# Kernel tuning notes

Measured on AMD Instinct MI355X. Metric: run time of the kernel, lower is better.

Reference implementation:

```python
import jax, jax.numpy as jnp
import numpy as np

NUM_HEADS = 16
LAMBDA = 0.1
HADAMARD_SCALE = 0.05
ROPE_BASE = 10000.0


def _rope(t):
    # t: [B, H, S, hd] -- rotary embedding (half-split convention)
    hd = t.shape[-1]
    S = t.shape[2]
    half = hd // 2
    inv_freq = 1.0 / (ROPE_BASE ** (jnp.arange(half, dtype=jnp.float32) / half))
    ang = jnp.arange(S, dtype=jnp.float32)[:, None] * inv_freq[None, :]  # [S, half]
    cos = jnp.cos(ang).astype(t.dtype)
    sin = jnp.sin(ang).astype(t.dtype)
    t1, t2 = t[..., :half], t[..., half:]
    return jnp.concatenate([t1 * cos - t2 * sin, t2 * cos + t1 * sin], axis=-1)


def _rotate_half(t):
    half = t.shape[-1] // 2
    return jnp.concatenate([-t[..., half:], t[..., :half]], axis=-1)


def setup_inputs() -> dict:
    key = jax.random.key(0)
    ks = jax.random.split(key, 6)
    B, S, D = 2, 2048, 1024
    scale = 1.0 / np.sqrt(D).astype(np.float32)
    x = jax.random.normal(ks[0], (B, S, D), jnp.float32)
    Wq = jax.random.normal(ks[1], (D, D), jnp.float32) * scale
    Wk = jax.random.normal(ks[2], (D, D), jnp.float32) * scale
    Wv = jax.random.normal(ks[3], (D, D), jnp.float32) * scale
    Wo = jax.random.normal(ks[4], (D, D), jnp.float32) * scale
    gate_w = jax.random.normal(ks[5], (D // NUM_HEADS,), jnp.float32) * 0.01
    return {"x": x, "Wq": Wq, "Wk": Wk, "Wv": Wv, "Wo": Wo, "gate_w": gate_w}


def reference(x, Wq, Wk, Wv, Wo, gate_w):
    B, S, D = x.shape
    H = NUM_HEADS
    hd = D // H

    def heads(W):
        return (x @ W.T).reshape(B, S, H, hd).transpose(0, 2, 1, 3)  # [B,H,S,hd]

    Q = _rope(heads(Wq))
    K = _rope(heads(Wk))
    V = heads(Wv)

    causal = jnp.tril(jnp.ones((S, S), dtype=bool))
    inv_sqrt_d = 1.0 / jnp.sqrt(jnp.asarray(hd, x.dtype))

    def attend(q, k):
        # first-order + lambda * second-order (elementwise-squared) scores
        s = (jnp.einsum('bhsd,bhtd->bhst', q, k)
             + LAMBDA * jnp.einsum('bhsd,bhtd->bhst', q * q, k * k)) * inv_sqrt_d
        s = jnp.where(causal, s, jnp.asarray(-1e9, s.dtype))
        a = jax.nn.softmax(s, axis=-1)
        return jnp.einsum('bhst,bhtd->bhsd', a, V)

    out1 = attend(Q, K)                                  # standard pass
    out2 = attend(_rotate_half(Q), _rotate_half(K))      # rotated second pass

    # hadamard gate mix of the two passes
    out = 0.5 * (out1 + out2) + HADAMARD_SCALE * (out1 * out2) * gate_w

    out = out.transpose(0, 2, 1, 3).reshape(B, S, D)
    return out @ Wo.T
```

## Files before the change

kernel.cpp:

```cpp
#include <hip/hip_runtime.h>

typedef unsigned short u16;
typedef __attribute__((ext_vector_type(4))) unsigned short u16x4;
typedef __attribute__((ext_vector_type(8))) unsigned short u16x8;
typedef __attribute__((ext_vector_type(8))) short s16x8;
typedef __attribute__((ext_vector_type(4))) float f32x4;

__device__ __forceinline__ u16 f2bf(float f) {
  unsigned int u = __float_as_uint(f);
  u += 0x7FFFu + ((u >> 16) & 1u);
  return (u16)(u >> 16);
}
__device__ __forceinline__ float bf2f(u16 h) {
  return __uint_as_float(((unsigned int)h) << 16);
}

__device__ __forceinline__ void gload_lds16(const u16* g, u16* l) {
  __builtin_amdgcn_global_load_lds(
      (const __attribute__((address_space(1))) unsigned int*)(g),
      (__attribute__((address_space(3))) unsigned int*)(l), 16, 0, 0);
}

__global__ __launch_bounds__(256) void cvt_all(const float* __restrict__ x,
                                               const float* __restrict__ Wq,
                                               const float* __restrict__ Wk,
                                               const float* __restrict__ Wv,
                                               const float* __restrict__ Wo,
                                               u16* __restrict__ xbf,
                                               u16* __restrict__ wbf,
                                               u16* __restrict__ wobf) {
  int blk = blockIdx.x;
  const float* src;
  u16* dst;
  int i;
  if (blk < 4096) {
    src = x; dst = xbf; i = blk * 256 + threadIdx.x;
  } else {
    int wb = blk - 4096;
    int sel = wb >> 10;
    src = (sel == 0) ? Wq : (sel == 1) ? Wk : (sel == 2) ? Wv : Wo;
    dst = (sel < 3) ? (wbf + (size_t)sel * 1048576) : wobf;
    i = (wb & 1023) * 256 + threadIdx.x;
  }
  float4 v = reinterpret_cast<const float4*>(src)[i];
  u16x4 o;
  o.x = f2bf(v.x); o.y = f2bf(v.y); o.z = f2bf(v.z); o.w = f2bf(v.w);
  reinterpret_cast<u16x4*>(dst)[i] = o;
}

__device__ __forceinline__ void store_out(float* p, float v) { *p = v; }
__device__ __forceinline__ void store_out(u16* p, float v) { *p = f2bf(v); }

template <typename OutT, int WM, int WN>
__global__ __launch_bounds__(256) void gemm_bt(const u16* __restrict__ A,
                                               const u16* __restrict__ Bw,
                                               OutT* __restrict__ C, int N, int K) {
  __shared__ u16 As[2][WM * 1024];
  __shared__ u16 Bs[2][WN * 1024];
  const int tid = threadIdx.x;
  const int lane = tid & 63;
  const int wave = tid >> 6;
  const int wm = wave >> 1, wn = wave & 1;
  const int lh = lane & 15, quad = lane >> 4;
  const int q8 = quad * 8;
  const int m0 = blockIdx.y * (WM * 32), n0 = blockIdx.x * (WN * 32);
  constexpr int NCH = 2 * (WM + WN);
  constexpr int PER = NCH / 4;

  auto stage = [&](int buf, int kt) {
    const int kb = kt * 32;
#pragma unroll
    for (int i = 0; i < PER; ++i) {
      const int c = wave * PER + i;
      if (c < 2 * WM) {
        gload_lds16(A + (size_t)(m0 + c * 16 + lh) * K + kb + q8,
                    &As[buf][c * 512 + lane * 8]);
      } else {
        const int rb = c - 2 * WM;
        gload_lds16(Bw + (size_t)(n0 + rb * 16 + lh) * K + kb + q8,
                    &Bs[buf][rb * 512 + lane * 8]);
      }
    }
  };

  f32x4 acc[WM][WN];
#pragma unroll
  for (int i = 0; i < WM; ++i)
#pragma unroll
    for (int j = 0; j < WN; ++j) { acc[i][j][0] = 0.f; acc[i][j][1] = 0.f; acc[i][j][2] = 0.f; acc[i][j][3] = 0.f; }

  const int nkt = K >> 5;
  stage(0, 0);
  __syncthreads();
  for (int kt = 0; kt < nkt; ++kt) {
    const int p = kt & 1;
    if (kt < nkt - 1) stage(1 - p, kt + 1);
    s16x8 af[WM], bf4[WN];
#pragma unroll
    for (int mb = 0; mb < WM; ++mb)
      af[mb] = *reinterpret_cast<const s16x8*>(&As[p][(wm * WM + mb) * 512 + lane * 8]);
#pragma unroll
    for (int nb = 0; nb < WN; ++nb)
      bf4[nb] = *reinterpret_cast<const s16x8*>(&Bs[p][(wn * WN + nb) * 512 + lane * 8]);
#pragma unroll
    for (int mb = 0; mb < WM; ++mb)
#pragma unroll
      for (int nb = 0; nb < WN; ++nb)
        acc[mb][nb] = __builtin_amdgcn_mfma_f32_16x16x32_bf16(af[mb], bf4[nb], acc[mb][nb], 0, 0, 0);
    __syncthreads();
  }
#pragma unroll
  for (int mb = 0; mb < WM; ++mb)
#pragma unroll
    for (int nb = 0; nb < WN; ++nb) {
      const int col = n0 + wn * (WN * 16) + nb * 16 + lh;
#pragma unroll
      for (int r = 0; r < 4; ++r) {
        const int row = m0 + wm * (WM * 16) + mb * 16 + quad * 4 + r;
        store_out(&C[(size_t)row * N + col], acc[mb][nb][r]);
      }
    }
}

__global__ __launch_bounds__(256) void qkv_gemm(const u16* __restrict__ A,
                                                const u16* __restrict__ Bw,
                                                u16* __restrict__ Vt,
                                                u16* __restrict__ Qs,
                                                u16* __restrict__ Kb,
                                                u16* __restrict__ K2b) {
  __shared__ u16 As[2][4096];
  __shared__ u16 Bs[2][4096];
  const int tid = threadIdx.x;
  const int lane = tid & 63;
  const int wave = tid >> 6;
  const int wm = wave >> 1, wn = wave & 1;
  const int lh = lane & 15, quad = lane >> 4;
  const int q8 = quad * 8;
  const int bx = blockIdx.x;
  const int m0 = blockIdx.y * 128, n0 = bx * 128;
  const int K = 1024;

  auto stage = [&](int buf, int kt) {
    const int kb = kt * 32;
#pragma unroll
    for (int i = 0; i < 4; ++i) {
      const int c = wave * 4 + i;
      if (c < 8) {
        gload_lds16(A + (size_t)(m0 + c * 16 + lh) * K + kb + q8,
                    &As[buf][c * 512 + lane * 8]);
      } else {
        const int rb = c - 8;
        gload_lds16(Bw + (size_t)(n0 + rb * 16 + lh) * K + kb + q8,
                    &Bs[buf][rb * 512 + lane * 8]);
      }
    }
  };

  f32x4 acc[4][4];
#pragma unroll
  for (int i = 0; i < 4; ++i)
#pragma unroll
    for (int j = 0; j < 4; ++j) { acc[i][j][0] = 0.f; acc[i][j][1] = 0.f; acc[i][j][2] = 0.f; acc[i][j][3] = 0.f; }

  stage(0, 0);
  __syncthreads();
  for (int kt = 0; kt < 32; ++kt) {
    const int p = kt & 1;
    if (kt < 31) stage(1 - p, kt + 1);
    s16x8 af[4], bf4[4];
#pragma unroll
    for (int mb = 0; mb < 4; ++mb)
      af[mb] = *reinterpret_cast<const s16x8*>(&As[p][(wm * 4 + mb) * 512 + lane * 8]);
#pragma unroll
    for (int nb = 0; nb < 4; ++nb)
      bf4[nb] = *reinterpret_cast<const s16x8*>(&Bs[p][(wn * 4 + nb) * 512 + lane * 8]);
#pragma unroll
    for (int mb = 0; mb < 4; ++mb)
#pragma unroll
      for (int nb = 0; nb < 4; ++nb)
        acc[mb][nb] = __builtin_amdgcn_mfma_f32_16x16x32_bf16(af[mb], bf4[nb], acc[mb][nb], 0, 0, 0);
    __syncthreads();
  }

  if (bx < 16) {
    const bool isQ = (bx < 8);
#pragma unroll
    for (int nb = 0; nb < 2; ++nb) {
      const int d = nb * 16 + lh;
      const float invf = __expf((float)d * -0.2878231366f);
      const int col = n0 + wn * 64 + nb * 16 + lh;
      const int ch = col & 1023;
      const int h = ch >> 6;
#pragma unroll
      for (int mb = 0; mb < 4; ++mb)
#pragma unroll
        for (int r = 0; r < 4; ++r) {
          const int row = m0 + wm * 64 + mb * 16 + quad * 4 + r;
          const int s = row & 2047, b = row >> 11;
          float ang = (float)s * invf;
          float sv, cv;
          __sincosf(ang, &sv, &cv);
          const float v1 = acc[mb][nb][r], v2 = acc[mb][nb + 2][r];
          const float e0 = v1 * cv - v2 * sv;
          const float e1 = v2 * cv + v1 * sv;
          const size_t ofs = (size_t)((b * 16 + h) * 2048 + s) * 64 + d;
          if (isQ) {
            Qs[ofs]      = f2bf(e0 * 0.125f);
            Qs[ofs + 32] = f2bf(e1 * 0.125f);
          } else {
            Kb[ofs]       = f2bf(e0);
            Kb[ofs + 32]  = f2bf(e1);
            K2b[ofs]      = f2bf(e0 * e0);
            K2b[ofs + 32] = f2bf(e1 * e1);
          }
        }
    }
  } else {
#pragma unroll
    for (int mb = 0; mb < 4; ++mb)
#pragma unroll
      for (int nb = 0; nb < 4; ++nb) {
        const int col = n0 + wn * 64 + nb * 16 + lh;
        const int ch = col & 1023;
        const int h = ch >> 6, d = ch & 63;
        const int row0 = m0 + wm * 64 + mb * 16 + quad * 4;
        const int s0 = row0 & 2047, b = row0 >> 11;
        u16x4 o;
#pragma unroll
        for (int r = 0; r < 4; ++r) o[r] = f2bf(acc[mb][nb][r]);
        *reinterpret_cast<u16x4*>(Vt + (size_t)((b * 16 + h) * 64 + d) * 2048 + s0) = o;
      }
  }
}

__global__ __launch_bounds__(256, 2) void attn_kernel(const u16* __restrict__ Qs,
                                                      const u16* __restrict__ Kb,
                                                      const u16* __restrict__ K2b,
                                                      const u16* __restrict__ Vt,
                                                      const float* __restrict__ gate,
                                                      u16* __restrict__ attn,
                                                      float* __restrict__ Opart,
                                                      float* __restrict__ Lpart,
                                                      float* __restrict__ Opart2,
                                                      float* __restrict__ Lpart2) {
  const int lin = blockIdx.y * 44 + blockIdx.x;
  const int xcd = lin & 7;
  const int slot = lin >> 3;
  const int bh = xcd * 4 + (slot / 44);
  const int bxv = slot % 44;

  int qi, kt0, kt1, chunk, which;
  bool split;
  if (bxv < 32) {
    qi = 15 - (bxv >> 2); chunk = bxv & 3; split = true; which = 0;
    const int T = 4 * qi + 4;
    kt0 = (chunk * T) >> 2;
    kt1 = (((chunk + 1) * T) >> 2) - 1;
  } else if (bxv < 40) {
    const int t = bxv - 32;
    qi = 7 - (t >> 1); chunk = t & 1; split = true; which = 1;
    const int nk = 2 * qi + 2; kt0 = chunk * nk; kt1 = kt0 + nk - 1;
  } else {
    qi = 43 - bxv; split = false; which = 0; chunk = 0; kt0 = 0; kt1 = 4 * qi + 3;
  }
  const int tid = threadIdx.x, lane = tid & 63, wave = tid >> 6;
  const int lh = lane & 15, quad = lane >> 4;
  const int b = bh >> 4, h = bh & 15;
  __shared__ u16 stageS[2][4096];
  __shared__ u16 Pbuf[4][640];
  const int base = qi * 128 + wave * 32;
  const int q8 = quad * 8;

  auto do_stage = [&](int buf, int kt) {
#pragma unroll
    for (int i = 0; i < 2; ++i) {
      const int c = wave * 2 + i;
      const int t2 = c >> 2, f = c & 3, kk = f >> 1, nb = f & 1;
      const u16* src = (t2 ? K2b : Kb) +
          (size_t)(bh * 2048 + kt * 32 + nb * 16 + lh) * 64 + kk * 32 + q8;
      gload_lds16(src, &stageS[buf][t2 * 2048 + f * 512 + lane * 8]);
    }
  };

  s16x8 qf[2][2], q2f[2][2];
#pragma unroll
  for (int mb = 0; mb < 2; ++mb) {
    const size_t qoff = (size_t)(bh * 2048 + base + mb * 16 + lh) * 64 + q8;
#pragma unroll
    for (int kk = 0; kk < 2; ++kk) {
      qf[mb][kk] = *reinterpret_cast<const s16x8*>(Qs + qoff + kk * 32);
#pragma unroll
      for (int j = 0; j < 8; ++j) {
        float f = bf2f((u16)qf[mb][kk][j]);
        q2f[mb][kk][j] = (short)f2bf(f * f * 0.8f);
      }
    }
  }

  const u16* Vbase = Vt + (size_t)bh * 131072;

  f32x4 oacc[2][4];
  float lsum[2][4];
#pragma unroll
  for (int mb = 0; mb < 2; ++mb)
#pragma unroll
    for (int nb = 0; nb < 4; ++nb) { oacc[mb][nb][0] = 0.f; oacc[mb][nb][1] = 0.f; oacc[mb][nb][2] = 0.f; oacc[mb][nb][3] = 0.f; }
#pragma unroll
  for (int mb = 0; mb < 2; ++mb)
#pragma unroll
    for (int r = 0; r < 4; ++r) lsum[mb][r] = 0.f;

  do_stage(0, kt0);
  __syncthreads();

  const int wmaxrow = base + 31;
  for (int kt = kt0; kt <= kt1; ++kt) {
    const int p = (kt - kt0) & 1;
    if (kt < kt1) do_stage(1 - p, kt + 1);

    if (kt * 32 <= wmaxrow) {
      const u16* Ks = stageS[p];
      f32x4 sacc[2][2];
#pragma unroll
      for (int mb = 0; mb < 2; ++mb)
#pragma unroll
        for (int nb = 0; nb < 2; ++nb) { sacc[mb][nb][0] = -8.f; sacc[mb][nb][1] = -8.f; sacc[mb][nb][2] = -8.f; sacc[mb][nb][3] = -8.f; }
      __builtin_amdgcn_s_setprio(1);
#pragma unroll
      for (int nb = 0; nb < 2; ++nb)
#pragma unroll
        for (int kk = 0; kk < 2; ++kk) {
          s16x8 kf  = *reinterpret_cast<const s16x8*>(&Ks[(kk * 2 + nb) * 512 + lane * 8]);
          s16x8 k2f = *reinterpret_cast<const s16x8*>(&Ks[2048 + (kk * 2 + nb) * 512 + lane * 8]);
#pragma unroll
          for (int mb = 0; mb < 2; ++mb) {
            sacc[mb][nb] = __builtin_amdgcn_mfma_f32_16x16x32_bf16(qf[mb][kk],  kf,  sacc[mb][nb], 0, 0, 0);
            sacc[mb][nb] = __builtin_amdgcn_mfma_f32_16x16x32_bf16(q2f[mb][kk], k2f, sacc[mb][nb], 0, 0, 0);
          }
        }
      __builtin_amdgcn_s_setprio(0);

      s16x8 vf[4];
#pragma unroll
      for (int nb = 0; nb < 4; ++nb)
        vf[nb] = *reinterpret_cast<const s16x8*>(
            Vbase + (size_t)(nb * 16 + lh) * 2048 + kt * 32 + q8);

      if (kt * 32 + 31 > base) {
#pragma unroll
        for (int mb = 0; mb < 2; ++mb)
#pragma unroll
          for (int nb = 0; nb < 2; ++nb) {
            const int colg = kt * 32 + nb * 16 + lh;
#pragma unroll
            for (int r = 0; r < 4; ++r) {
              const int rowg = base + mb * 16 + quad * 4 + r;
              if (colg > rowg) sacc[mb][nb][r] = -1e9f;
            }
          }
      }
#pragma unroll
      for (int mb = 0; mb < 2; ++mb) {
#pragma unroll
        for (int nb = 0; nb < 2; ++nb)
#pragma unroll
          for (int r = 0; r < 4; ++r) {
            float pv = __expf(sacc[mb][nb][r]);
            lsum[mb][r] += pv;
            Pbuf[wave][(quad * 4 + r) * 40 + nb * 16 + lh] = f2bf(pv);
          }
        s16x8 pf = *reinterpret_cast<const s16x8*>(&Pbuf[wave][lh * 40 + q8]);
        __builtin_amdgcn_s_setprio(1);
#pragma unroll
        for (int nb = 0; nb < 4; ++nb)
          oacc[mb][nb] = __builtin_amdgcn_mfma_f32_16x16x32_bf16(pf, vf[nb], oacc[mb][nb], 0, 0, 0);
        __builtin_amdgcn_s_setprio(0);
      }
    }
    __syncthreads();
  }
#pragma unroll
  for (int mb = 0; mb < 2; ++mb)
#pragma unroll
    for (int r = 0; r < 4; ++r) {
      float rs = lsum[mb][r];
#pragma unroll
      for (int off = 1; off < 16; off <<= 1) rs += __shfl_xor(rs, off);
      lsum[mb][r] = rs;
    }
  if (split) {
#pragma unroll
    for (int mb = 0; mb < 2; ++mb)
#pragma unroll
      for (int r = 0; r < 4; ++r) {
        const int rowg = base + mb * 16 + quad * 4 + r;
        if (which == 0) {
          const size_t orow = (size_t)chunk * 32768 + bh * 1024 + (rowg - 1024);
          if (lh == 0) Lpart[orow] = lsum[mb][r];
#pragma unroll
          for (int nb = 0; nb < 4; ++nb)
            Opart[orow * 64 + nb * 16 + lh] = oacc[mb][nb][r];
        } else {
          const size_t orow = (size_t)chunk * 16384 + bh * 512 + (rowg - 512);
          if (lh == 0) Lpart2[orow] = lsum[mb][r];
#pragma unroll
          for (int nb = 0; nb < 4; ++nb)
            Opart2[orow * 64 + nb * 16 + lh] = oacc[mb][nb][r];
        }
      }
  } else {
#pragma unroll
    for (int mb = 0; mb < 2; ++mb)
#pragma unroll
      for (int r = 0; r < 4; ++r) {
        const float invl = 1.0f / lsum[mb][r];
        const int rows = base + mb * 16 + quad * 4 + r;
#pragma unroll
        for (int nb = 0; nb < 4; ++nb) {
          float o = oacc[mb][nb][r] * invl;
          float val = o + 0.05f * o * o * gate[nb * 16 + lh];
          attn[(size_t)(b * 2048 + rows) * 1024 + h * 64 + nb * 16 + lh] = f2bf(val);
        }
      }
  }
}

__global__ __launch_bounds__(256) void combine_kernel(const float* __restrict__ Opart,
                                                      const float* __restrict__ Lpart,
                                                      const float* __restrict__ Opart2,
                                                      const float* __restrict__ Lpart2,
                                                      const float* __restrict__ gate,
                                                      u16* __restrict__ attn) {
  int idx = blockIdx.x * 256 + threadIdx.x;
  int d = idx & 63;
  int r_all = idx >> 6;
  float o, l;
  int bh, s;
  if (r_all < 32768) {
    o = Opart[idx] + Opart[idx + 2097152] + Opart[idx + 4194304] + Opart[idx + 6291456];
    l = Lpart[r_all] + Lpart[r_all + 32768] + Lpart[r_all + 65536] + Lpart[r_all + 98304];
    bh = r_all >> 10; s = 1024 + (r_all & 1023);
  } else {
    const int r2 = r_all - 32768;
    const int i2 = idx - 2097152;
    o = Opart2[i2] + Opart2[i2 + 1048576];
    l = Lpart2[r2] + Lpart2[r2 + 16384];
    bh = r2 >> 9; s = 512 + (r2 & 511);
  }
  o /= l;
  float val = o + 0.05f * o * o * gate[d];
  int b = bh >> 4, h = bh & 15;
  attn[(size_t)(b * 2048 + s) * 1024 + h * 64 + d] = f2bf(val);
}

extern "C" void kernel_launch(void* const* d_in, const int* in_sizes, int n_in,
                              void* d_out, int out_size, void* d_ws, size_t ws_size,
                              hipStream_t stream) {
  (void)in_sizes; (void)n_in; (void)out_size; (void)ws_size;
  const float* x    = (const float*)d_in[0];
  const float* Wq   = (const float*)d_in[1];
  const float* Wk   = (const float*)d_in[2];
  const float* Wv   = (const float*)d_in[3];
  const float* Wo   = (const float*)d_in[4];
  const float* gate = (const float*)d_in[5];

  u16* ws    = (u16*)d_ws;
  u16* xbf   = ws;
  u16* wbf   = xbf + 4194304;
  u16* wobf  = wbf + 3145728;
  u16* Qsb   = wobf + 1048576;
  u16* Kbb   = Qsb + 4194304;
  u16* K2bb  = Kbb + 4194304;
  u16* Vtb   = K2bb + 4194304;
  float* Opart  = (float*)(Vtb + 4194304);
  float* Lpart  = Opart + 8388608;
  float* Opart2 = Lpart + 131072;
  float* Lpart2 = Opart2 + 2097152;
  u16* attnb = xbf;

  cvt_all<<<8192, 256, 0, stream>>>(x, Wq, Wk, Wv, Wo, xbf, wbf, wobf);
  qkv_gemm<<<dim3(24, 32), 256, 0, stream>>>(xbf, wbf, Vtb, Qsb, Kbb, K2bb);
  attn_kernel<<<dim3(44, 32), 256, 0, stream>>>(Qsb, Kbb, K2bb, Vtb, gate, attnb,
                                                Opart, Lpart, Opart2, Lpart2);
  combine_kernel<<<12288, 256, 0, stream>>>(Opart, Lpart, Opart2, Lpart2, gate, attnb);
  gemm_bt<float, 4, 2><<<dim3(16, 32), 256, 0, stream>>>(attnb, wobf, (float*)d_out, 1024, 1024);
}
```

Measured before the change: 242.3 us.

## Software-pipeline PV MFMA one tile behind QK and remap GEMM blocks per XCD

The attention loop now defers the P·V MFMAs of each key tile to the next iteration. It double-buffers P in LDS per wave and prefetches V fragments a tile ahead, so the exp/softmax VALU work and the global V loads overlap with the next tile's QK MFMAs. Separately, the GEMM and QKV GEMM kernels remap linear block IDs so that consecutive row-tiles land on the same XCD, to improve L2 reuse of A rows. The costs are more LDS (4x Pbuf), extra live registers for vfp, and a drain step after the loop.

```diff
diff --git a/kernel.cpp b/kernel.cpp
--- a/kernel.cpp
+++ b/kernel.cpp
@@ -63,7 +63,15 @@
   const int wm = wave >> 1, wn = wave & 1;
   const int lh = lane & 15, quad = lane >> 4;
   const int q8 = quad * 8;
-  const int m0 = blockIdx.y * (WM * 32), n0 = blockIdx.x * (WN * 32);
+  int vbx = blockIdx.x, vby = blockIdx.y;
+  if ((gridDim.y & 7) == 0) {
+    const int W = gridDim.x;
+    const int lin = blockIdx.y * W + blockIdx.x;
+    const int xcd = lin & 7, slot = lin >> 3;
+    vbx = slot % W;
+    vby = xcd * (gridDim.y >> 3) + slot / W;
+  }
+  const int m0 = vby * (WM * 32), n0 = vbx * (WN * 32);
   constexpr int NCH = 2 * (WM + WN);
   constexpr int PER = NCH / 4;
 
@@ -136,8 +144,11 @@
   const int wm = wave >> 1, wn = wave & 1;
   const int lh = lane & 15, quad = lane >> 4;
   const int q8 = quad * 8;
-  const int bx = blockIdx.x;
-  const int m0 = blockIdx.y * 128, n0 = bx * 128;
+  const int lin = blockIdx.y * 24 + blockIdx.x;
+  const int xcd = lin & 7, slot = lin >> 3;
+  const int bx = slot % 24;
+  const int vby = xcd * 4 + slot / 24;
+  const int m0 = vby * 128, n0 = bx * 128;
   const int K = 1024;
 
   auto stage = [&](int buf, int kt) {
@@ -267,7 +278,7 @@
   const int lh = lane & 15, quad = lane >> 4;
   const int b = bh >> 4, h = bh & 15;
   __shared__ u16 stageS[2][4096];
-  __shared__ u16 Pbuf[4][640];
+  __shared__ u16 Pbuf[4][2][2][640];
   const int base = qi * 128 + wave * 32;
   const int q8 = quad * 8;
 
@@ -313,6 +324,10 @@
   do_stage(0, kt0);
   __syncthreads();
 
+  s16x8 vfp[4];
+  int pvalid = 0;
+  int pendp = 0;
+
   const int wmaxrow = base + 31;
   for (int kt = kt0; kt <= kt1; ++kt) {
     const int p = (kt - kt0) & 1;
@@ -338,13 +353,16 @@
             sacc[mb][nb] = __builtin_amdgcn_mfma_f32_16x16x32_bf16(q2f[mb][kk], k2f, sacc[mb][nb], 0, 0, 0);
           }
         }
+      if (pvalid) {
+#pragma unroll
+        for (int mb = 0; mb < 2; ++mb) {
+          s16x8 pf = *reinterpret_cast<const s16x8*>(&Pbuf[wave][pendp][mb][lh * 40 + q8]);
+#pragma unroll
+          for (int nb = 0; nb < 4; ++nb)
+            oacc[mb][nb] = __builtin_amdgcn_mfma_f32_16x16x32_bf16(pf, vfp[nb], oacc[mb][nb], 0, 0, 0);
+        }
+      }
       __builtin_amdgcn_s_setprio(0);
-
-      s16x8 vf[4];
-#pragma unroll
-      for (int nb = 0; nb < 4; ++nb)
-        vf[nb] = *reinterpret_cast<const s16x8*>(
-            Vbase + (size_t)(nb * 16 + lh) * 2048 + kt * 32 + q8);
 
       if (kt * 32 + 31 > base) {
 #pragma unroll
@@ -360,24 +378,31 @@
           }
       }
 #pragma unroll
-      for (int mb = 0; mb < 2; ++mb) {
+      for (int mb = 0; mb < 2; ++mb)
 #pragma unroll
         for (int nb = 0; nb < 2; ++nb)
 #pragma unroll
           for (int r = 0; r < 4; ++r) {
             float pv = __expf(sacc[mb][nb][r]);
             lsum[mb][r] += pv;
-            Pbuf[wave][(quad * 4 + r) * 40 + nb * 16 + lh] = f2bf(pv);
+            Pbuf[wave][p][mb][(quad * 4 + r) * 40 + nb * 16 + lh] = f2bf(pv);
           }
-        s16x8 pf = *reinterpret_cast<const s16x8*>(&Pbuf[wave][lh * 40 + q8]);
-        __builtin_amdgcn_s_setprio(1);
-#pragma unroll
-        for (int nb = 0; nb < 4; ++nb)
-          oacc[mb][nb] = __builtin_amdgcn_mfma_f32_16x16x32_bf16(pf, vf[nb], oacc[mb][nb], 0, 0, 0);
-        __builtin_amdgcn_s_setprio(0);
-      }
+#pragma unroll
+      for (int nb = 0; nb < 4; ++nb)
+        vfp[nb] = *reinterpret_cast<const s16x8*>(
+            Vbase + (size_t)(nb * 16 + lh) * 2048 + kt * 32 + q8);
+      pvalid = 1; pendp = p;
     }
     __syncthreads();
+  }
+  if (pvalid) {
+#pragma unroll
+    for (int mb = 0; mb < 2; ++mb) {
+      s16x8 pf = *reinterpret_cast<const s16x8*>(&Pbuf[wave][pendp][mb][lh * 40 + q8]);
+#pragma unroll
+      for (int nb = 0; nb < 4; ++nb)
+        oacc[mb][nb] = __builtin_amdgcn_mfma_f32_16x16x32_bf16(pf, vfp[nb], oacc[mb][nb], 0, 0, 0);
+    }
   }
 #pragma unroll
   for (int mb = 0; mb < 2; ++mb)
```

Result: no change. 240.2 us (-0.9%).

## Compute transposed attention scores to keep P in registers; add XCD-aware GEMM block remap

Applied to the files above, without the earlier changes.

The attention kernel now computes S^T (keys as MFMA rows, queries as columns). The exp'd probabilities then land directly in the register layout the PV MFMA expects, which removes the per-wave LDS round trip through Pbuf. V fragments are loaded as two 4-element pieces so their k-ordering matches the new P layout, and the row sums are reduced with fewer shuffles. Separately, the GEMM and QKV kernels remap block indices so that consecutive blocks on each XCD share A rows, aiming for better L2 reuse. The cost is narrower V loads (8-byte instead of 16-byte) and an extra shuffle in the epilogue.

```diff
diff --git a/kernel.cpp b/kernel.cpp
--- a/kernel.cpp
+++ b/kernel.cpp
@@ -3,6 +3,7 @@
 typedef unsigned short u16;
 typedef __attribute__((ext_vector_type(4))) unsigned short u16x4;
 typedef __attribute__((ext_vector_type(8))) unsigned short u16x8;
+typedef __attribute__((ext_vector_type(4))) short s16x4;
 typedef __attribute__((ext_vector_type(8))) short s16x8;
 typedef __attribute__((ext_vector_type(4))) float f32x4;
 
@@ -63,7 +64,15 @@
   const int wm = wave >> 1, wn = wave & 1;
   const int lh = lane & 15, quad = lane >> 4;
   const int q8 = quad * 8;
-  const int m0 = blockIdx.y * (WM * 32), n0 = blockIdx.x * (WN * 32);
+  int vbx = blockIdx.x, vby = blockIdx.y;
+  if ((gridDim.y & 7) == 0) {
+    const int W = gridDim.x;
+    const int lin = blockIdx.y * W + blockIdx.x;
+    const int xcd = lin & 7, slot = lin >> 3;
+    vbx = slot % W;
+    vby = xcd * (gridDim.y >> 3) + slot / W;
+  }
+  const int m0 = vby * (WM * 32), n0 = vbx * (WN * 32);
   constexpr int NCH = 2 * (WM + WN);
   constexpr int PER = NCH / 4;
 
@@ -136,8 +145,11 @@
   const int wm = wave >> 1, wn = wave & 1;
   const int lh = lane & 15, quad = lane >> 4;
   const int q8 = quad * 8;
-  const int bx = blockIdx.x;
-  const int m0 = blockIdx.y * 128, n0 = bx * 128;
+  const int lin = blockIdx.y * 24 + blockIdx.x;
+  const int xcd = lin & 7, slot = lin >> 3;
+  const int bx = slot % 24;
+  const int vby = xcd * 4 + slot / 24;
+  const int m0 = vby * 128, n0 = bx * 128;
   const int K = 1024;
 
   auto stage = [&](int buf, int kt) {
@@ -267,7 +279,6 @@
   const int lh = lane & 15, quad = lane >> 4;
   const int b = bh >> 4, h = bh & 15;
   __shared__ u16 stageS[2][4096];
-  __shared__ u16 Pbuf[4][640];
   const int base = qi * 128 + wave * 32;
   const int q8 = quad * 8;
 
@@ -275,24 +286,24 @@
 #pragma unroll
     for (int i = 0; i < 2; ++i) {
       const int c = wave * 2 + i;
-      const int t2 = c >> 2, f = c & 3, kk = f >> 1, nb = f & 1;
+      const int t2 = c >> 2, f = c & 3, kk = f >> 1, kb2 = f & 1;
       const u16* src = (t2 ? K2b : Kb) +
-          (size_t)(bh * 2048 + kt * 32 + nb * 16 + lh) * 64 + kk * 32 + q8;
+          (size_t)(bh * 2048 + kt * 32 + kb2 * 16 + lh) * 64 + kk * 32 + q8;
       gload_lds16(src, &stageS[buf][t2 * 2048 + f * 512 + lane * 8]);
     }
   };
 
   s16x8 qf[2][2], q2f[2][2];
 #pragma unroll
-  for (int mb = 0; mb < 2; ++mb) {
-    const size_t qoff = (size_t)(bh * 2048 + base + mb * 16 + lh) * 64 + q8;
+  for (int qb = 0; qb < 2; ++qb) {
+    const size_t qoff = (size_t)(bh * 2048 + base + qb * 16 + lh) * 64 + q8;
 #pragma unroll
     for (int kk = 0; kk < 2; ++kk) {
-      qf[mb][kk] = *reinterpret_cast<const s16x8*>(Qs + qoff + kk * 32);
+      qf[qb][kk] = *reinterpret_cast<const s16x8*>(Qs + qoff + kk * 32);
 #pragma unroll
       for (int j = 0; j < 8; ++j) {
-        float f = bf2f((u16)qf[mb][kk][j]);
-        q2f[mb][kk][j] = (short)f2bf(f * f * 0.8f);
+        float f = bf2f((u16)qf[qb][kk][j]);
+        q2f[qb][kk][j] = (short)f2bf(f * f * 0.8f);
       }
     }
   }
@@ -300,15 +311,13 @@
   const u16* Vbase = Vt + (size_t)bh * 131072;
 
   f32x4 oacc[2][4];
-  float lsum[2][4];
-#pragma unroll
-  for (int mb = 0; mb < 2; ++mb)
-#pragma unroll
-    for (int nb = 0; nb < 4; ++nb) { oacc[mb][nb][0] = 0.f; oacc[mb][nb][1] = 0.f; oacc[mb][nb][2] = 0.f; oacc[mb][nb][3] = 0.f; }
-#pragma unroll
-  for (int mb = 0; mb < 2; ++mb)
-#pragma unroll
-    for (int r = 0; r < 4; ++r) lsum[mb][r] = 0.f;
+  float lsum[2];
+#pragma unroll
+  for (int qb = 0; qb < 2; ++qb) {
+#pragma unroll
+    for (int nb = 0; nb < 4; ++nb) { oacc[qb][nb][0] = 0.f; oacc[qb][nb][1] = 0.f; oacc[qb][nb][2] = 0.f; oacc[qb][nb][3] = 0.f; }
+    lsum[qb] = 0.f;
+  }
 
   do_stage(0, kt0);
   __syncthreads();
@@ -322,102 +331,107 @@
       const u16* Ks = stageS[p];
       f32x4 sacc[2][2];
 #pragma unroll
-      for (int mb = 0; mb < 2; ++mb)
-#pragma unroll
-        for (int nb = 0; nb < 2; ++nb) { sacc[mb][nb][0] = -8.f; sacc[mb][nb][1] = -8.f; sacc[mb][nb][2] = -8.f; sacc[mb][nb][3] = -8.f; }
+      for (int kb = 0; kb < 2; ++kb)
+#pragma unroll
+        for (int qb = 0; qb < 2; ++qb) { sacc[kb][qb][0] = -8.f; sacc[kb][qb][1] = -8.f; sacc[kb][qb][2] = -8.f; sacc[kb][qb][3] = -8.f; }
       __builtin_amdgcn_s_setprio(1);
 #pragma unroll
-      for (int nb = 0; nb < 2; ++nb)
+      for (int kb = 0; kb < 2; ++kb)
 #pragma unroll
         for (int kk = 0; kk < 2; ++kk) {
-          s16x8 kf  = *reinterpret_cast<const s16x8*>(&Ks[(kk * 2 + nb) * 512 + lane * 8]);
-          s16x8 k2f = *reinterpret_cast<const s16x8*>(&Ks[2048 + (kk * 2 + nb) * 512 + lane * 8]);
-#pragma unroll
-          for (int mb = 0; mb < 2; ++mb) {
-            sacc[mb][nb] = __builtin_amdgcn_mfma_f32_16x16x32_bf16(qf[mb][kk],  kf,  sacc[mb][nb], 0, 0, 0);
-            sacc[mb][nb] = __builtin_amdgcn_mfma_f32_16x16x32_bf16(q2f[mb][kk], k2f, sacc[mb][nb], 0, 0, 0);
+          s16x8 kf  = *reinterpret_cast<const s16x8*>(&Ks[(kk * 2 + kb) * 512 + lane * 8]);
+          s16x8 k2f = *reinterpret_cast<const s16x8*>(&Ks[2048 + (kk * 2 + kb) * 512 + lane * 8]);
+#pragma unroll
+          for (int qb = 0; qb < 2; ++qb) {
+            sacc[kb][qb] = __builtin_amdgcn_mfma_f32_16x16x32_bf16(kf,  qf[qb][kk],  sacc[kb][qb], 0, 0, 0);
+            sacc[kb][qb] = __builtin_amdgcn_mfma_f32_16x16x32_bf16(k2f, q2f[qb][kk], sacc[kb][qb], 0, 0, 0);
           }
         }
       __builtin_amdgcn_s_setprio(0);
 
       s16x8 vf[4];
 #pragma unroll
-      for (int nb = 0; nb < 4; ++nb)
-        vf[nb] = *reinterpret_cast<const s16x8*>(
-            Vbase + (size_t)(nb * 16 + lh) * 2048 + kt * 32 + q8);
+      for (int nb = 0; nb < 4; ++nb) {
+        const u16* vrow = Vbase + (size_t)(nb * 16 + lh) * 2048 + kt * 32 + quad * 4;
+        s16x4 lo = *reinterpret_cast<const s16x4*>(vrow);
+        s16x4 hi = *reinterpret_cast<const s16x4*>(vrow + 16);
+        vf[nb][0] = lo[0]; vf[nb][1] = lo[1]; vf[nb][2] = lo[2]; vf[nb][3] = lo[3];
+        vf[nb][4] = hi[0]; vf[nb][5] = hi[1]; vf[nb][6] = hi[2]; vf[nb][7] = hi[3];
+      }
 
       if (kt * 32 + 31 > base) {
 #pragma unroll
-        for (int mb = 0; mb < 2; ++mb)
-#pragma unroll
-          for (int nb = 0; nb < 2; ++nb) {
-            const int colg = kt * 32 + nb * 16 + lh;
+        for (int kb = 0; kb < 2; ++kb)
+#pragma unroll
+          for (int qb = 0; qb < 2; ++qb) {
+            const int queryg = base + qb * 16 + lh;
 #pragma unroll
             for (int r = 0; r < 4; ++r) {
-              const int rowg = base + mb * 16 + quad * 4 + r;
-              if (colg > rowg) sacc[mb][nb][r] = -1e9f;
+              const int keyg = kt * 32 + kb * 16 + quad * 4 + r;
+              if (keyg > queryg) sacc[kb][qb][r] = -1e9f;
             }
           }
       }
-#pragma unroll
-      for (int mb = 0; mb < 2; ++mb) {
-#pragma unroll
-        for (int nb = 0; nb < 2; ++nb)
+      s16x8 pa[2];
+#pragma unroll
+      for (int qb = 0; qb < 2; ++qb)
+#pragma unroll
+        for (int kb = 0; kb < 2; ++kb)
 #pragma unroll
           for (int r = 0; r < 4; ++r) {
-            float pv = __expf(sacc[mb][nb][r]);
-            lsum[mb][r] += pv;
-            Pbuf[wave][(quad * 4 + r) * 40 + nb * 16 + lh] = f2bf(pv);
+            float pv = __expf(sacc[kb][qb][r]);
+            lsum[qb] += pv;
+            pa[qb][kb * 4 + r] = (short)f2bf(pv);
           }
-        s16x8 pf = *reinterpret_cast<const s16x8*>(&Pbuf[wave][lh * 40 + q8]);
-        __builtin_amdgcn_s_setprio(1);
+      __builtin_amdgcn_s_setprio(1);
+#pragma unroll
+      for (int qb = 0; qb < 2; ++qb)
 #pragma unroll
         for (int nb = 0; nb < 4; ++nb)
-          oacc[mb][nb] = __builtin_amdgcn_mfma_f32_16x16x32_bf16(pf, vf[nb], oacc[mb][nb], 0, 0, 0);
-        __builtin_amdgcn_s_setprio(0);
-      }
+          oacc[qb][nb] = __builtin_amdgcn_mfma_f32_16x16x32_bf16(pa[qb], vf[nb], oacc[qb][nb], 0, 0, 0);
+      __builtin_amdgcn_s_setprio(0);
     }
     __syncthreads();
   }
 #pragma unroll
-  for (int mb = 0; mb < 2; ++mb)
-#pragma unroll
-    for (int r = 0; r < 4; ++r) {
-      float rs = lsum[mb][r];
-#pragma unroll
-      for (int off = 1; off < 16; off <<= 1) rs += __shfl_xor(rs, off);
-      lsum[mb][r] = rs;
-    }
+  for (int qb = 0; qb < 2; ++qb) {
+    float rs = lsum[qb];
+    rs += __shfl_xor(rs, 16);
+    rs += __shfl_xor(rs, 32);
+    lsum[qb] = rs;
+  }
   if (split) {
 #pragma unroll
-    for (int mb = 0; mb < 2; ++mb)
+    for (int qb = 0; qb < 2; ++qb)
 #pragma unroll
       for (int r = 0; r < 4; ++r) {
-        const int rowg = base + mb * 16 + quad * 4 + r;
+        const float lq = __shfl(lsum[qb], quad * 4 + r);
+        const int rowg = base + qb * 16 + quad * 4 + r;
         if (which == 0) {
           const size_t orow = (size_t)chunk * 32768 + bh * 1024 + (rowg - 1024);
-          if (lh == 0) Lpart[orow] = lsum[mb][r];
+          if (lh == 0) Lpart[orow] = lq;
 #pragma unroll
           for (int nb = 0; nb < 4; ++nb)
-            Opart[orow * 64 + nb * 16 + lh] = oacc[mb][nb][r];
+            Opart[orow * 64 + nb * 16 + lh] = oacc[qb][nb][r];
         } else {
           const size_t orow = (size_t)chunk * 16384 + bh * 512 + (rowg - 512);
-          if (lh == 0) Lpart2[orow] = lsum[mb][r];
+          if (lh == 0) Lpart2[orow] = lq;
 #pragma unroll
           for (int nb = 0; nb < 4; ++nb)
-            Opart2[orow * 64 + nb * 16 + lh] = oacc[mb][nb][r];
+            Opart2[orow * 64 + nb * 16 + lh] = oacc[qb][nb][r];
         }
       }
   } else {
 #pragma unroll
-    for (int mb = 0; mb < 2; ++mb)
+    for (int qb = 0; qb < 2; ++qb)
 #pragma unroll
       for (int r = 0; r < 4; ++r) {
-        const float invl = 1.0f / lsum[mb][r];
-        const int rows = base + mb * 16 + quad * 4 + r;
+        const float lq = __shfl(lsum[qb], quad * 4 + r);
+        const float invl = 1.0f / lq;
+        const int rows = base + qb * 16 + quad * 4 + r;
 #pragma unroll
         for (int nb = 0; nb < 4; ++nb) {
-          float o = oacc[mb][nb][r] * invl;
+          float o = oacc[qb][nb][r] * invl;
           float val = o + 0.05f * o * o * gate[nb * 16 + lh];
           attn[(size_t)(b * 2048 + rows) * 1024 + h * 64 + nb * 16 + lh] = f2bf(val);
         }
```

Result: slower. 279.0 us (+15.1%).
